# Optimization experiments

Hardware: AMD Instinct MI355X
Metric: run time of the kernel (lower is better)

Reference implementation:

```python
import jax, jax.numpy as jnp
import numpy as np

HIDDEN = 3072
HEADS = 24
HEAD_DIM = HIDDEN // HEADS  # 128
MLP_HIDDEN = 4 * HIDDEN     # 12288
IMG_LEN = 1024
TXT_LEN = 256
L = IMG_LEN + TXT_LEN
B = 1
EPS = 1e-6


def setup_inputs() -> dict:
    key = jax.random.key(0)
    ks = jax.random.split(key, 12)
    x = jax.random.normal(ks[0], (B, L, HIDDEN), jnp.float32)
    vec = jax.random.normal(ks[1], (B, HIDDEN), jnp.float32)
    # RoPE tables: real cos/sin of position * inv_freq, repeated over pairs (full head_dim)
    inv_freq = 1.0 / (10000.0 ** (np.arange(0, HEAD_DIM, 2, dtype=np.float32) / HEAD_DIM))
    theta = np.arange(IMG_LEN, dtype=np.float32)[:, None] * inv_freq[None, :]  # [img_len, D/2]
    theta = np.repeat(theta, 2, axis=-1)  # [img_len, D]
    freqs_cos = jnp.asarray(np.cos(theta))[None, :, None, :]  # [1, img_len, 1, D]
    freqs_sin = jnp.asarray(np.sin(theta))[None, :, None, :]
    s = 0.02
    mod_w = jax.random.normal(ks[2], (HIDDEN, 3 * HIDDEN), jnp.float32) * s
    mod_b = jnp.zeros((3 * HIDDEN,), jnp.float32)
    w1 = jax.random.normal(ks[3], (HIDDEN, 3 * HIDDEN + MLP_HIDDEN), jnp.float32) * s
    b1 = jnp.zeros((3 * HIDDEN + MLP_HIDDEN,), jnp.float32)
    w2 = jax.random.normal(ks[4], (HIDDEN + MLP_HIDDEN, HIDDEN), jnp.float32) * s
    b2 = jnp.zeros((HIDDEN,), jnp.float32)
    qn_w = jnp.ones((HEAD_DIM,), jnp.float32)
    kn_w = jnp.ones((HEAD_DIM,), jnp.float32)
    cu_seqlens_q = jnp.array([0, IMG_LEN, L], jnp.int32)
    cu_seqlens_kv = jnp.array([0, IMG_LEN, L], jnp.int32)
    return {"x": x, "vec": vec, "freqs_cos": freqs_cos, "freqs_sin": freqs_sin,
            "mod_w": mod_w, "mod_b": mod_b, "w1": w1, "b1": b1, "w2": w2, "b2": b2,
            "qn_w": qn_w, "kn_w": kn_w, "img_len": IMG_LEN,
            "cu_seqlens_q": cu_seqlens_q, "cu_seqlens_kv": cu_seqlens_kv}


def _layernorm(x):  # elementwise_affine=False
    mu = jnp.mean(x, axis=-1, keepdims=True)
    var = jnp.mean(jnp.square(x - mu), axis=-1, keepdims=True)
    return (x - mu) * jax.lax.rsqrt(var + EPS)


def _rmsnorm(x, w):
    ms = jnp.mean(jnp.square(x), axis=-1, keepdims=True)
    return x * jax.lax.rsqrt(ms + EPS) * w


def _rope_interleaved(x, cos, sin):
    # mode=1: rotate interleaved pairs: (-x1, x0, -x3, x2, ...)
    x0 = x[..., 0::2]
    x1 = x[..., 1::2]
    rot = jnp.stack([-x1, x0], axis=-1).reshape(x.shape)
    return x * cos + rot * sin


def reference(x, vec, freqs_cos, freqs_sin, mod_w, mod_b, w1, b1, w2, b2,
              qn_w, kn_w, img_len, cu_seqlens_q, cu_seqlens_kv):
    bs = x.shape[0]
    assert cu_seqlens_q.shape[0] == 2 * bs + 1
    # adaLN modulation: SiLU -> Linear(hidden, 3*hidden)
    mod = jax.nn.silu(vec) @ mod_w + mod_b           # [B, 3H]
    mod = mod[:, None, :]                             # [B, 1, 3H]
    mod_shift, mod_scale, mod_gate = jnp.split(mod, 3, axis=-1)
    x_mod = _layernorm(x) * (1.0 + mod_scale) + mod_shift
    # fused QKV + MLP projection
    h = x_mod @ w1 + b1                               # [B, L, 3*hidden + mlp]
    qkv = h[..., :3 * HIDDEN]
    mlp = h[..., 3 * HIDDEN:]
    # 'B L (K H D) -> K B L H D'
    qkv = qkv.reshape(bs, -1, 3, HEADS, HEAD_DIM)
    q, k, v = qkv[:, :, 0], qkv[:, :, 1], qkv[:, :, 2]  # [B, L, H, D]
    q = _rmsnorm(q, qn_w)
    k = _rmsnorm(k, kn_w)
    # RoPE on image tokens only
    img_q = _rope_interleaved(q[:, :img_len], freqs_cos, freqs_sin)
    img_k = _rope_interleaved(k[:, :img_len], freqs_cos, freqs_sin)
    q = jnp.concatenate([img_q, q[:, img_len:]], axis=1)
    k = jnp.concatenate([img_k, k[:, img_len:]], axis=1)
    # dense attention (bs==1 path, no mask), scale = 1/sqrt(head_dim)
    scale = 1.0 / jnp.sqrt(jnp.float32(HEAD_DIM))
    scores = jnp.einsum('bqhd,bkhd->bhqk', q, k) * scale
    probs = jax.nn.softmax(scores, axis=-1)
    attn = jnp.einsum('bhqk,bkhd->bqhd', probs, v)
    attn = attn.reshape(bs, -1, HEADS * HEAD_DIM)     # [B, L, hidden]
    # output projection on concat(attn, gelu_tanh(mlp))
    out = jnp.concatenate([attn, jax.nn.gelu(mlp, approximate=True)], axis=-1) @ w2 + b2
    return x + out * mod_gate
```

## Files before the change

kernel.cpp:

```cpp
#include <hip/hip_runtime.h>
#include <cstdint>
#include <cstddef>

typedef __bf16 bf16x8_t __attribute__((ext_vector_type(8)));
typedef float f32x4 __attribute__((ext_vector_type(4)));

#define HID 3072
#define NHEADS 24
#define HD 128
#define MLP 12288
#define SEQ 1280
#define IMG 1024
#define N1 21504
#define QKVW 9216
#define A2W 15360
#define EPSV 1e-6f

__device__ __forceinline__ size_t tpos(int row, int col, int KT) {
    return ((size_t)(row >> 8) * KT + (col >> 6)) * 16384
         + (size_t)(((((col >> 5) & 1) << 4) + ((row >> 4) & 15)) * 512
                    + (((row & 15) + (((col >> 3) & 3) << 4)) << 3) + (col & 7));
}

__device__ __forceinline__ void gload16(const void* g, void* l) {
    __builtin_amdgcn_global_load_lds(
        (const __attribute__((address_space(1))) unsigned int*)g,
        (__attribute__((address_space(3))) unsigned int*)l, 16, 0, 0);
}

__device__ __forceinline__ void bar() {
    asm volatile("" ::: "memory");
    __builtin_amdgcn_s_barrier();
    asm volatile("" ::: "memory");
}

__global__ void silu_kernel(const float* __restrict__ v, float* __restrict__ sv) {
    int i = blockIdx.x * 256 + threadIdx.x;
    float x = v[i];
    sv[i] = x / (1.f + expf(-x));
}

__global__ void gemv_part(const float* __restrict__ sv, const float* __restrict__ W,
                          float* __restrict__ part) {
    int n = blockIdx.x * 256 + threadIdx.x;
    int k0 = blockIdx.y * 384;
    float s = 0.f;
    for (int k = k0; k < k0 + 384; ++k)
        s = fmaf(sv[k], W[(size_t)k * QKVW + n], s);
    part[(size_t)blockIdx.y * QKVW + n] = s;
}

__global__ void gemv_reduce(const float* __restrict__ part, const float* __restrict__ bias,
                            float* __restrict__ mod) {
    int n = blockIdx.x * 256 + threadIdx.x;
    float s = bias[n];
    #pragma unroll
    for (int ky = 0; ky < 8; ++ky) s += part[(size_t)ky * QKVW + n];
    mod[n] = s;
}

__global__ __launch_bounds__(384) void ln_mod_kernel(const float* __restrict__ x,
                                                     const float* __restrict__ mod,
                                                     ushort* __restrict__ xmt) {
    int m = blockIdx.x;
    int t = threadIdx.x;
    int lane = t & 63, w = t >> 6;
    const float* xr = x + (size_t)m * HID;
    float4 v0 = *reinterpret_cast<const float4*>(&xr[t * 8]);
    float4 v1 = *reinterpret_cast<const float4*>(&xr[t * 8 + 4]);
    float s = v0.x + v0.y + v0.z + v0.w + v1.x + v1.y + v1.z + v1.w;
    float sq = v0.x * v0.x + v0.y * v0.y + v0.z * v0.z + v0.w * v0.w +
               v1.x * v1.x + v1.y * v1.y + v1.z * v1.z + v1.w * v1.w;
    #pragma unroll
    for (int off = 1; off < 64; off <<= 1) {
        s += __shfl_xor(s, off);
        sq += __shfl_xor(sq, off);
    }
    __shared__ float red[12];
    if (lane == 0) { red[w] = s; red[w + 6] = sq; }
    __syncthreads();
    s = red[0] + red[1] + red[2] + red[3] + red[4] + red[5];
    sq = red[6] + red[7] + red[8] + red[9] + red[10] + red[11];
    float mu = s * (1.f / HID);
    float var = sq * (1.f / HID) - mu * mu;
    float rs = rsqrtf(var + EPSV);
    float vals[8] = {v0.x, v0.y, v0.z, v0.w, v1.x, v1.y, v1.z, v1.w};
    union { ushort u[8]; uint4 q; } pk;
    #pragma unroll
    for (int j = 0; j < 8; ++j) {
        int n = t * 8 + j;
        float y = (vals[j] - mu) * rs * (1.f + mod[HID + n]) + mod[n];
        pk.u[j] = __builtin_bit_cast(ushort, (__bf16)y);
    }
    *reinterpret_cast<uint4*>(&xmt[tpos(m, t * 8, HID >> 6)]) = pk.q;
}

__global__ __launch_bounds__(256) void convB_kernel(const float* __restrict__ in,
                                                    ushort* __restrict__ out, int K, int N) {
    __shared__ float tle[64][65];
    int KT = K >> 6;
    int kb = blockIdx.x % KT, nb = blockIdx.x / KT;
    int k0 = kb * 64, n0 = nb * 64;
    int tid = threadIdx.x;
    int rr = tid >> 2, cg = (tid & 3) * 16;
    #pragma unroll
    for (int j = 0; j < 4; ++j) {
        float4 vv = *reinterpret_cast<const float4*>(&in[(size_t)(k0 + rr) * N + n0 + cg + j * 4]);
        tle[rr][cg + j * 4 + 0] = vv.x;
        tle[rr][cg + j * 4 + 1] = vv.y;
        tle[rr][cg + j * 4 + 2] = vv.z;
        tle[rr][cg + j * 4 + 3] = vv.w;
    }
    __syncthreads();
    int nl = tid & 63;
    #pragma unroll
    for (int gg = 0; gg < 2; ++gg) {
        int g = (tid >> 6) + gg * 4;
        union { ushort u[8]; uint4 q; } pk;
        #pragma unroll
        for (int j = 0; j < 8; ++j)
            pk.u[j] = __builtin_bit_cast(ushort, (__bf16)tle[g * 8 + j][nl]);
        *reinterpret_cast<uint4*>(&out[tpos(n0 + nl, k0 + g * 8, KT)]) = pk.q;
    }
}

template <int EPI, int SPLITS>
__global__ __launch_bounds__(512, 2) void gemm8p(
    const ushort* __restrict__ At, const ushort* __restrict__ Bt,
    const float* __restrict__ bias, float* __restrict__ outf, ushort* __restrict__ outb,
    int KTtot, int NTloc, int NTN) {
    int nwg = gridDim.x;
    int q = nwg >> 3, r = nwg & 7;
    int orig = blockIdx.x;
    int xcd = orig & 7;
    int wgid = (xcd < r ? xcd * (q + 1) : r * (q + 1) + (xcd - r) * q) + (orig >> 3);
    int mt = wgid % 5;
    int p = wgid / 5;
    int nt = p % NTN;
    int sp = p / NTN;
    int kOff = sp * NTloc;
    int m0 = mt * 256, n0 = nt * 256;

    __shared__ ushort LA[2][16384];
    __shared__ ushort LB[2][16384];

    int tid = threadIdx.x;
    int lane = tid & 63, wid = tid >> 6;
    int wm = wid >> 2, wn = wid & 3;
    int lr = lane & 15, lg = lane >> 4;

    const ushort* gA = At + (size_t)mt * KTtot * 16384;
    const ushort* gB = Bt + (size_t)nt * KTtot * 16384;

    f32x4 acc[8][4] = {};
    bf16x8_t af[4][2], bf0[2][2], bf1[2][2];

    auto stageA = [&](int buf, int ktG, int h) {
        #pragma unroll
        for (int j = 0; j < 2; ++j) {
            int sidx = wid * 2 + j;
            int b = h * 8 + ((sidx & 8) ? 16 + (sidx & 7) : (sidx & 7));
            gload16(gA + (size_t)ktG * 16384 + b * 512 + lane * 8, &LA[buf][b * 512]);
        }
    };
    auto stageB = [&](int buf, int ktG, int h) {
        #pragma unroll
        for (int j = 0; j < 2; ++j) {
            int sidx = wid * 2 + j;
            int b = h * 8 + ((sidx & 8) ? 16 + (sidx & 7) : (sidx & 7));
            gload16(gB + (size_t)ktG * 16384 + b * 512 + lane * 8, &LB[buf][b * 512]);
        }
    };
    auto rdA = [&](int buf, int h) {
        #pragma unroll
        for (int mi = 0; mi < 4; ++mi)
            #pragma unroll
            for (int k = 0; k < 2; ++k)
                af[mi][k] = *reinterpret_cast<const bf16x8_t*>(
                    &LA[buf][(k * 16 + wm * 8 + h * 4 + mi) * 512 + lane * 8]);
    };
    auto rdB = [&](int buf, int v, bf16x8_t bf[2][2]) {
        #pragma unroll
        for (int ni = 0; ni < 2; ++ni)
            #pragma unroll
            for (int k = 0; k < 2; ++k)
                bf[ni][k] = *reinterpret_cast<const bf16x8_t*>(
                    &LB[buf][(k * 16 + wn * 4 + v * 2 + ni) * 512 + lane * 8]);
    };
    auto mm = [&](int h, int v, bf16x8_t bf[2][2]) {
        __builtin_amdgcn_s_setprio(1);
        #pragma unroll
        for (int mi = 0; mi < 4; ++mi)
            #pragma unroll
            for (int ni = 0; ni < 2; ++ni)
                #pragma unroll
                for (int k = 0; k < 2; ++k)
                    acc[h * 4 + mi][v * 2 + ni] = __builtin_amdgcn_mfma_f32_16x16x32_bf16(
                        af[mi][k], bf[ni][k], acc[h * 4 + mi][v * 2 + ni], 0, 0, 0);
        __builtin_amdgcn_s_setprio(0);
    };

    stageB(0, kOff, 0);
    stageB(0, kOff, 1);
    stageA(0, kOff, 0);
    stageA(0, kOff, 1);
    if (NTloc > 1) stageB(1, kOff + 1, 0);

    for (int t = 0; t < NTloc; ++t) {
        int c = t & 1;
        bool pf1 = (t + 1 < NTloc);
        if (pf1) {
            stageB(c ^ 1, kOff + t + 1, 1);
            asm volatile("s_waitcnt vmcnt(4)" ::: "memory");
        } else {
            asm volatile("s_waitcnt vmcnt(0)" ::: "memory");
        }
        bar();
        rdA(c, 0);
        rdB(c, 0, bf0);
        mm(0, 0, bf0);
        bar();
        rdB(c, 1, bf1);
        if (pf1) stageA(c ^ 1, kOff + t + 1, 0);
        mm(0, 1, bf1);
        bar();
        rdA(c, 1);
        if (pf1) stageA(c ^ 1, kOff + t + 1, 1);
        mm(1, 0, bf0);
        bar();
        if (t + 2 < NTloc) stageB(c, kOff + t + 2, 0);
        mm(1, 1, bf1);
        bar();
    }

    #pragma unroll
    for (int mi8 = 0; mi8 < 8; ++mi8) {
        #pragma unroll
        for (int nj = 0; nj < 4; ++nj) {
            int col = n0 + wn * 64 + nj * 16 + lr;
            #pragma unroll
            for (int rr2 = 0; rr2 < 4; ++rr2) {
                int row = m0 + wm * 128 + mi8 * 16 + lg * 4 + rr2;
                float val = acc[mi8][nj][rr2];
                if (EPI == 1) {
                    val += bias[col];
                    if (n0 < QKVW) {
                        outf[(size_t)row * QKVW + col] = val;
                    } else {
                        float u = 0.7978845608028654f * (val + 0.044715f * val * val * val);
                        float g = val / (1.f + __expf(-2.f * u));
                        outb[tpos(row, HID + (col - QKVW), A2W >> 6)] =
                            __builtin_bit_cast(ushort, (__bf16)g);
                    }
                } else {
                    outf[(size_t)(sp * SEQ + row) * HID + col] = val;
                }
            }
        }
    }
}

__global__ __launch_bounds__(256) void ksplit_reduce(const float* __restrict__ part,
                                                     const float* __restrict__ x,
                                                     const float* __restrict__ bias,
                                                     const float* __restrict__ gate,
                                                     float* __restrict__ out) {
    int i = blockIdx.x * 256 + threadIdx.x;
    int col = (i % (HID / 4)) * 4;
    f32x4 a = *reinterpret_cast<const f32x4*>(&part[(size_t)i * 4]);
    #pragma unroll
    for (int s = 1; s < 4; ++s) {
        f32x4 p = *reinterpret_cast<const f32x4*>(&part[(size_t)s * SEQ * HID + (size_t)i * 4]);
        #pragma unroll
        for (int c = 0; c < 4; ++c) a[c] += p[c];
    }
    f32x4 xv = *reinterpret_cast<const f32x4*>(&x[(size_t)i * 4]);
    f32x4 bv = *reinterpret_cast<const f32x4*>(&bias[col]);
    f32x4 gv = *reinterpret_cast<const f32x4*>(&gate[col]);
    f32x4 o;
    #pragma unroll
    for (int c = 0; c < 4; ++c) o[c] = xv[c] + (a[c] + bv[c]) * gv[c];
    *reinterpret_cast<f32x4*>(&out[(size_t)i * 4]) = o;
}

__global__ __launch_bounds__(256) void qkv_post(const float* __restrict__ h,
                                                const float* __restrict__ fc,
                                                const float* __restrict__ fs,
                                                const float* __restrict__ qn,
                                                const float* __restrict__ kn,
                                                __bf16* __restrict__ qb,
                                                __bf16* __restrict__ kb,
                                                __bf16* __restrict__ vb) {
    int m = blockIdx.x;
    int lane = threadIdx.x & 63, w = threadIdx.x >> 6;
    for (int rr = w; rr < 72; rr += 4) {
        int s = rr / 24, hd = rr % 24;
        const float* src = h + (size_t)m * QKVW + s * HID + hd * HD;
        float2 xv = *reinterpret_cast<const float2*>(&src[2 * lane]);
        float x0 = xv.x, x1 = xv.y;
        if (s < 2) {
            float ss = x0 * x0 + x1 * x1;
            #pragma unroll
            for (int off = 1; off < 64; off <<= 1) ss += __shfl_xor(ss, off);
            float rs = rsqrtf(ss * (1.f / HD) + EPSV);
            const float* nw = (s == 0) ? qn : kn;
            x0 *= rs * nw[2 * lane];
            x1 *= rs * nw[2 * lane + 1];
            if (m < IMG) {
                float c0 = fc[m * HD + 2 * lane], c1 = fc[m * HD + 2 * lane + 1];
                float s0 = fs[m * HD + 2 * lane], s1 = fs[m * HD + 2 * lane + 1];
                float r0 = x0 * c0 - x1 * s0;
                float r1 = x1 * c1 + x0 * s1;
                x0 = r0; x1 = r1;
            }
        }
        __bf16* dst = ((s == 0) ? qb : (s == 1) ? kb : vb) + (size_t)hd * SEQ * HD + (size_t)m * HD + 2 * lane;
        ushort u0 = __builtin_bit_cast(ushort, (__bf16)x0);
        ushort u1 = __builtin_bit_cast(ushort, (__bf16)x1);
        *reinterpret_cast<uint*>(dst) = (uint)u0 | ((uint)u1 << 16);
    }
}

__global__ __launch_bounds__(256) void attn_kernel(const __bf16* __restrict__ qb,
                                                   const __bf16* __restrict__ kb,
                                                   const __bf16* __restrict__ vb,
                                                   ushort* __restrict__ a2) {
    int head = blockIdx.y;
    int tid = threadIdx.x;
    int lane = tid & 63, w = tid >> 6;
    int lr = lane & 15, lg = lane >> 4;
    int q0 = blockIdx.x * 64 + w * 16;
    const __bf16* Q = qb + (size_t)head * SEQ * HD;
    const __bf16* Kp = kb + (size_t)head * SEQ * HD;
    const __bf16* Vp = vb + (size_t)head * SEQ * HD;

    bf16x8_t qf[4];
    #pragma unroll
    for (int kc = 0; kc < 4; ++kc)
        qf[kc] = *reinterpret_cast<const bf16x8_t*>(&Q[(size_t)(q0 + lr) * HD + kc * 32 + lg * 8]);

    __shared__ alignas(16) __bf16 Kl[32][136];
    __shared__ alignas(16) __bf16 Vl[32][136];
    __shared__ float Pl[4][32][16];

    float m_run = -1e30f, l_run = 0.f;
    f32x4 of[8] = {};
    const float sm_scale = 0.08838834764831845f;

    for (int kv0 = 0; kv0 < SEQ; kv0 += 32) {
        #pragma unroll
        for (int cc = 0; cc < 2; ++cc) {
            int c = tid + cc * 256;
            int row = c >> 4, off = (c & 15) * 8;
            *reinterpret_cast<bf16x8_t*>(&Kl[row][off]) =
                *reinterpret_cast<const bf16x8_t*>(&Kp[(size_t)(kv0 + row) * HD + off]);
            *reinterpret_cast<bf16x8_t*>(&Vl[row][off]) =
                *reinterpret_cast<const bf16x8_t*>(&Vp[(size_t)(kv0 + row) * HD + off]);
        }
        __syncthreads();

        f32x4 st[2] = {};
        #pragma unroll
        for (int h = 0; h < 2; ++h)
            #pragma unroll
            for (int kc = 0; kc < 4; ++kc) {
                bf16x8_t kf = *reinterpret_cast<const bf16x8_t*>(&Kl[h * 16 + lr][kc * 32 + lg * 8]);
                st[h] = __builtin_amdgcn_mfma_f32_16x16x32_bf16(kf, qf[kc], st[h], 0, 0, 0);
            }
        float sarr[8];
        #pragma unroll
        for (int h = 0; h < 2; ++h)
            #pragma unroll
            for (int r = 0; r < 4; ++r) sarr[h * 4 + r] = st[h][r] * sm_scale;

        float mloc = sarr[0];
        #pragma unroll
        for (int i = 1; i < 8; ++i) mloc = fmaxf(mloc, sarr[i]);
        mloc = fmaxf(mloc, __shfl_xor(mloc, 16));
        mloc = fmaxf(mloc, __shfl_xor(mloc, 32));
        float m_new = fmaxf(m_run, mloc);
        float alpha = expf(m_run - m_new);
        float pv[8], psum = 0.f;
        #pragma unroll
        for (int i = 0; i < 8; ++i) { pv[i] = expf(sarr[i] - m_new); psum += pv[i]; }
        psum += __shfl_xor(psum, 16);
        psum += __shfl_xor(psum, 32);
        l_run = l_run * alpha + psum;
        m_run = m_new;

        #pragma unroll
        for (int h = 0; h < 2; ++h)
            #pragma unroll
            for (int r = 0; r < 4; ++r) Pl[w][h * 16 + lg * 4 + r][lr] = pv[h * 4 + r];
        bf16x8_t pa;
        #pragma unroll
        for (int j = 0; j < 8; ++j) pa[j] = (__bf16)Pl[w][lg * 8 + j][lr];

        float alr[4];
        #pragma unroll
        for (int r = 0; r < 4; ++r) alr[r] = __shfl(alpha, lg * 4 + r);

        #pragma unroll
        for (int db = 0; db < 8; ++db) {
            #pragma unroll
            for (int r = 0; r < 4; ++r) of[db][r] *= alr[r];
            bf16x8_t vv;
            #pragma unroll
            for (int j = 0; j < 8; ++j) vv[j] = Vl[lg * 8 + j][db * 16 + lr];
            of[db] = __builtin_amdgcn_mfma_f32_16x16x32_bf16(pa, vv, of[db], 0, 0, 0);
        }
        __syncthreads();
    }

    float lr4[4];
    #pragma unroll
    for (int r = 0; r < 4; ++r) lr4[r] = __shfl(l_run, lg * 4 + r);
    #pragma unroll
    for (int db = 0; db < 8; ++db)
        #pragma unroll
        for (int r = 0; r < 4; ++r) {
            int row = q0 + lg * 4 + r;
            int col = head * HD + db * 16 + lr;
            a2[tpos(row, col, A2W >> 6)] =
                __builtin_bit_cast(ushort, (__bf16)(of[db][r] / lr4[r]));
        }
}

extern "C" void kernel_launch(void* const* d_in, const int* in_sizes, int n_in,
                              void* d_out, int out_size, void* d_ws, size_t ws_size,
                              hipStream_t stream) {
    const float* x = (const float*)d_in[0];
    const float* vec = (const float*)d_in[1];
    const float* fc = (const float*)d_in[2];
    const float* fs = (const float*)d_in[3];
    const float* mod_w = (const float*)d_in[4];
    const float* mod_b = (const float*)d_in[5];
    const float* w1 = (const float*)d_in[6];
    const float* b1 = (const float*)d_in[7];
    const float* w2 = (const float*)d_in[8];
    const float* b2 = (const float*)d_in[9];
    const float* qn = (const float*)d_in[10];
    const float* kn = (const float*)d_in[11];
    float* out = (float*)d_out;

    char* ws = (char*)d_ws;
    size_t off = 0;
    float* sv = (float*)(ws + off); off += 3072 * 4;
    float* mod = (float*)(ws + off); off += 9216 * 4;
    float* part = (float*)(ws + off); off += 8 * 9216 * 4;
    off = (off + 255) & ~(size_t)255;
    ushort* xmt = (ushort*)(ws + off); off += (size_t)SEQ * HID * 2;
    off = (off + 255) & ~(size_t)255;
    float* hqkv = (float*)(ws + off); off += (size_t)SEQ * QKVW * 4;
    __bf16* qb = (__bf16*)(ws + off); off += (size_t)NHEADS * SEQ * HD * 2;
    __bf16* kb = (__bf16*)(ws + off); off += (size_t)NHEADS * SEQ * HD * 2;
    __bf16* vb = (__bf16*)(ws + off); off += (size_t)NHEADS * SEQ * HD * 2;
    off = (off + 255) & ~(size_t)255;
    ushort* a2t = (ushort*)(ws + off); off += (size_t)SEQ * A2W * 2;
    float* part2 = hqkv;

    off = (off + 255) & ~(size_t)255;
    ushort* w1b = (ushort*)(ws + off);
    ushort* w2b = w1b;

    silu_kernel<<<12, 256, 0, stream>>>(vec, sv);
    gemv_part<<<dim3(36, 8), 256, 0, stream>>>(sv, mod_w, part);
    gemv_reduce<<<36, 256, 0, stream>>>(part, mod_b, mod);
    ln_mod_kernel<<<SEQ, 384, 0, stream>>>(x, mod, xmt);

    convB_kernel<<<(HID / 64) * (N1 / 64), 256, 0, stream>>>(w1, w1b, HID, N1);
    gemm8p<1, 1><<<5 * (N1 / 256), 512, 0, stream>>>(xmt, w1b, b1, hqkv, a2t,
                                                     HID / 64, HID / 64, N1 / 256);
    convB_kernel<<<(A2W / 64) * (HID / 64), 256, 0, stream>>>(w2, w2b, A2W, HID);
    qkv_post<<<SEQ, 256, 0, stream>>>(hqkv, fc, fs, qn, kn, qb, kb, vb);
    attn_kernel<<<dim3(SEQ / 64, NHEADS), 256, 0, stream>>>(qb, kb, vb, a2t);
    gemm8p<2, 4><<<4 * 5 * (HID / 256), 512, 0, stream>>>(a2t, w2b, nullptr, part2, nullptr,
                                                          A2W / 64, A2W / 64 / 4, HID / 256);
    ksplit_reduce<<<SEQ * HID / 1024, 256, 0, stream>>>(part2, x, b2, mod + 2 * HID, out);
}
```

Baseline: 684.5 us.

## Restructure GEMM main loop with deeper prefetch and register double-buffered fragments

```diff
diff --git a/kernel.cpp b/kernel.cpp
--- a/kernel.cpp
+++ b/kernel.cpp
@@ -153,25 +153,16 @@
     const ushort* gB = Bt + (size_t)nt * KTtot * 16384;
 
     f32x4 acc[8][4] = {};
-    bf16x8_t af[4][2], bf0[2][2], bf1[2][2];
-
-    auto stageA = [&](int buf, int ktG, int h) {
-        #pragma unroll
-        for (int j = 0; j < 2; ++j) {
-            int sidx = wid * 2 + j;
-            int b = h * 8 + ((sidx & 8) ? 16 + (sidx & 7) : (sidx & 7));
-            gload16(gA + (size_t)ktG * 16384 + b * 512 + lane * 8, &LA[buf][b * 512]);
+    bf16x8_t af0[4][2], af1[4][2], bf0[2][2], bf1[2][2];
+
+    auto stage = [&](ushort (*L)[16384], int buf, const ushort* g, int ktG) {
+        #pragma unroll
+        for (int j = 0; j < 4; ++j) {
+            int b = wid * 4 + j;
+            gload16(g + (size_t)ktG * 16384 + b * 512 + lane * 8, &L[buf][b * 512]);
         }
     };
-    auto stageB = [&](int buf, int ktG, int h) {
-        #pragma unroll
-        for (int j = 0; j < 2; ++j) {
-            int sidx = wid * 2 + j;
-            int b = h * 8 + ((sidx & 8) ? 16 + (sidx & 7) : (sidx & 7));
-            gload16(gB + (size_t)ktG * 16384 + b * 512 + lane * 8, &LB[buf][b * 512]);
-        }
-    };
-    auto rdA = [&](int buf, int h) {
+    auto rdA = [&](int buf, int h, bf16x8_t (&af)[4][2]) {
         #pragma unroll
         for (int mi = 0; mi < 4; ++mi)
             #pragma unroll
@@ -179,7 +170,7 @@
                 af[mi][k] = *reinterpret_cast<const bf16x8_t*>(
                     &LA[buf][(k * 16 + wm * 8 + h * 4 + mi) * 512 + lane * 8]);
     };
-    auto rdB = [&](int buf, int v, bf16x8_t bf[2][2]) {
+    auto rdB = [&](int buf, int v, bf16x8_t (&bf)[2][2]) {
         #pragma unroll
         for (int ni = 0; ni < 2; ++ni)
             #pragma unroll
@@ -187,7 +178,7 @@
                 bf[ni][k] = *reinterpret_cast<const bf16x8_t*>(
                     &LB[buf][(k * 16 + wn * 4 + v * 2 + ni) * 512 + lane * 8]);
     };
-    auto mm = [&](int h, int v, bf16x8_t bf[2][2]) {
+    auto mmq = [&](bf16x8_t (&af)[4][2], bf16x8_t (&bf)[2][2], int h, int v) {
         __builtin_amdgcn_s_setprio(1);
         #pragma unroll
         for (int mi = 0; mi < 4; ++mi)
@@ -200,36 +191,36 @@
         __builtin_amdgcn_s_setprio(0);
     };
 
-    stageB(0, kOff, 0);
-    stageB(0, kOff, 1);
-    stageA(0, kOff, 0);
-    stageA(0, kOff, 1);
-    if (NTloc > 1) stageB(1, kOff + 1, 0);
+    stage(LA, 0, gA, kOff);
+    stage(LB, 0, gB, kOff);
+    stage(LA, 1, gA, kOff + 1);
+    stage(LB, 1, gB, kOff + 1);
+    asm volatile("s_waitcnt vmcnt(8)" ::: "memory");
+    bar();
+    rdA(0, 0, af0);
+    rdB(0, 0, bf0);
 
     for (int t = 0; t < NTloc; ++t) {
         int c = t & 1;
-        bool pf1 = (t + 1 < NTloc);
-        if (pf1) {
-            stageB(c ^ 1, kOff + t + 1, 1);
-            asm volatile("s_waitcnt vmcnt(4)" ::: "memory");
-        } else {
-            asm volatile("s_waitcnt vmcnt(0)" ::: "memory");
-        }
+        rdB(c, 1, bf1);
+        mmq(af0, bf0, 0, 0);
         bar();
-        rdA(c, 0);
-        rdB(c, 0, bf0);
-        mm(0, 0, bf0);
+        rdA(c, 1, af1);
+        mmq(af0, bf1, 0, 1);
         bar();
-        rdB(c, 1, bf1);
-        if (pf1) stageA(c ^ 1, kOff + t + 1, 0);
-        mm(0, 1, bf1);
+        if (t + 2 < NTloc) stage(LA, c, gA, kOff + t + 2);
+        mmq(af1, bf0, 1, 0);
+        if (t + 1 < NTloc) {
+            if (t + 2 < NTloc) asm volatile("s_waitcnt vmcnt(4)" ::: "memory");
+            else               asm volatile("s_waitcnt vmcnt(0)" ::: "memory");
+        }
         bar();
-        rdA(c, 1);
-        if (pf1) stageA(c ^ 1, kOff + t + 1, 1);
-        mm(1, 0, bf0);
-        bar();
-        if (t + 2 < NTloc) stageB(c, kOff + t + 2, 0);
-        mm(1, 1, bf1);
+        if (t + 1 < NTloc) {
+            rdA(c ^ 1, 0, af0);
+            rdB(c ^ 1, 0, bf0);
+        }
+        if (t + 2 < NTloc) stage(LB, c, gB, kOff + t + 2);
+        mmq(af1, bf1, 1, 1);
         bar();
     }
 
```

Result: faster. 653.7 us (-4.5%).

## Deepen GEMM global-to-LDS prefetch pipeline and fence LDS reads before MFMA

Applied to the files above, without the earlier changes.

```diff
diff --git a/kernel.cpp b/kernel.cpp
--- a/kernel.cpp
+++ b/kernel.cpp
@@ -33,6 +33,9 @@
     __builtin_amdgcn_s_barrier();
     asm volatile("" ::: "memory");
 }
+
+#define LGKM0 do { asm volatile("s_waitcnt lgkmcnt(0)" ::: "memory"); \
+                   __builtin_amdgcn_sched_barrier(0); } while (0)
 
 __global__ void silu_kernel(const float* __restrict__ v, float* __restrict__ sv) {
     int i = blockIdx.x * 256 + threadIdx.x;
@@ -155,20 +158,11 @@
     f32x4 acc[8][4] = {};
     bf16x8_t af[4][2], bf0[2][2], bf1[2][2];
 
-    auto stageA = [&](int buf, int ktG, int h) {
+    auto stage2 = [&](ushort (*L)[16384], int buf, const ushort* g, int ktG, int half) {
         #pragma unroll
         for (int j = 0; j < 2; ++j) {
-            int sidx = wid * 2 + j;
-            int b = h * 8 + ((sidx & 8) ? 16 + (sidx & 7) : (sidx & 7));
-            gload16(gA + (size_t)ktG * 16384 + b * 512 + lane * 8, &LA[buf][b * 512]);
-        }
-    };
-    auto stageB = [&](int buf, int ktG, int h) {
-        #pragma unroll
-        for (int j = 0; j < 2; ++j) {
-            int sidx = wid * 2 + j;
-            int b = h * 8 + ((sidx & 8) ? 16 + (sidx & 7) : (sidx & 7));
-            gload16(gB + (size_t)ktG * 16384 + b * 512 + lane * 8, &LB[buf][b * 512]);
+            int b = wid * 4 + half * 2 + j;
+            gload16(g + (size_t)ktG * 16384 + b * 512 + lane * 8, &L[buf][b * 512]);
         }
     };
     auto rdA = [&](int buf, int h) {
@@ -179,7 +173,7 @@
                 af[mi][k] = *reinterpret_cast<const bf16x8_t*>(
                     &LA[buf][(k * 16 + wm * 8 + h * 4 + mi) * 512 + lane * 8]);
     };
-    auto rdB = [&](int buf, int v, bf16x8_t bf[2][2]) {
+    auto rdB = [&](int buf, int v, bf16x8_t (&bf)[2][2]) {
         #pragma unroll
         for (int ni = 0; ni < 2; ++ni)
             #pragma unroll
@@ -187,7 +181,7 @@
                 bf[ni][k] = *reinterpret_cast<const bf16x8_t*>(
                     &LB[buf][(k * 16 + wn * 4 + v * 2 + ni) * 512 + lane * 8]);
     };
-    auto mm = [&](int h, int v, bf16x8_t bf[2][2]) {
+    auto mmq = [&](bf16x8_t (&bf)[2][2], int h, int v) {
         __builtin_amdgcn_s_setprio(1);
         #pragma unroll
         for (int mi = 0; mi < 4; ++mi)
@@ -200,36 +194,41 @@
         __builtin_amdgcn_s_setprio(0);
     };
 
-    stageB(0, kOff, 0);
-    stageB(0, kOff, 1);
-    stageA(0, kOff, 0);
-    stageA(0, kOff, 1);
-    if (NTloc > 1) stageB(1, kOff + 1, 0);
+    stage2(LA, 0, gA, kOff, 0); stage2(LA, 0, gA, kOff, 1);
+    stage2(LB, 0, gB, kOff, 0); stage2(LB, 0, gB, kOff, 1);
+    if (NTloc > 1) {
+        stage2(LB, 1, gB, kOff + 1, 0); stage2(LB, 1, gB, kOff + 1, 1);
+        stage2(LA, 1, gA, kOff + 1, 0);
+    }
+    asm volatile("s_waitcnt vmcnt(6)" ::: "memory");
+    bar();
 
     for (int t = 0; t < NTloc; ++t) {
         int c = t & 1;
         bool pf1 = (t + 1 < NTloc);
-        if (pf1) {
-            stageB(c ^ 1, kOff + t + 1, 1);
-            asm volatile("s_waitcnt vmcnt(4)" ::: "memory");
-        } else {
-            asm volatile("s_waitcnt vmcnt(0)" ::: "memory");
-        }
-        bar();
+        bool pf2 = (t + 2 < NTloc);
+        if (pf1) stage2(LA, c ^ 1, gA, kOff + t + 1, 1);
         rdA(c, 0);
         rdB(c, 0, bf0);
-        mm(0, 0, bf0);
+        bar(); LGKM0;
+        mmq(bf0, 0, 0);
         bar();
         rdB(c, 1, bf1);
-        if (pf1) stageA(c ^ 1, kOff + t + 1, 0);
-        mm(0, 1, bf1);
+        bar(); LGKM0;
+        mmq(bf1, 0, 1);
         bar();
+        if (pf2) stage2(LB, c, gB, kOff + t + 2, 0);
         rdA(c, 1);
-        if (pf1) stageA(c ^ 1, kOff + t + 1, 1);
-        mm(1, 0, bf0);
+        bar(); LGKM0;
+        mmq(bf0, 1, 0);
         bar();
-        if (t + 2 < NTloc) stageB(c, kOff + t + 2, 0);
-        mm(1, 1, bf1);
+        if (pf2) { stage2(LB, c, gB, kOff + t + 2, 1); stage2(LA, c, gA, kOff + t + 2, 0); }
+        if (pf1) {
+            if (pf2) asm volatile("s_waitcnt vmcnt(6)" ::: "memory");
+            else     asm volatile("s_waitcnt vmcnt(0)" ::: "memory");
+        }
+        bar();
+        mmq(bf1, 1, 1);
         bar();
     }
 
```

After: 705.5 us. +3.1%, slower.
